# Optimization experiments

Hardware: AMD Instinct MI355X
Metric: run time of the kernel (lower is better)

## Reference

```python
import jax, jax.numpy as jnp
import numpy as np

STRIDE = 1

def setup_inputs() -> dict:
    key = jax.random.key(0)
    k1, k2 = jax.random.split(key)
    x = jax.random.normal(k1, (16, 32, 32768), dtype=jnp.float32)
    # original uses torch.rand -> uniform [0,1)
    kernel = jax.random.uniform(k2, (1, 32, 32, 3), dtype=jnp.float32)
    return {"x": x, "kernel": kernel}

def reference(x, kernel):
    # Faithful intent of the module: strided valid 1D convolution.
    # x: (B, C_in, L); kernel: (1, C_out, C_in, K)
    w = kernel[0]  # (C_out, C_in, K)
    out = jax.lax.conv_general_dilated(
        x, w,
        window_strides=(STRIDE,),
        padding='VALID',
        dimension_numbers=('NCH', 'OIH', 'NCH'),
    )  # (B, C_out, (L-K)//STRIDE + 1)
    return out
```

## Files before the change

### kernel.cpp

```cpp
#include <hip/hip_runtime.h>

#define L_IN   32768
#define L_OUT  32766
#define C_IN   32
#define C_OUT  32
#define KW     3
#define TILE_L 256
#define XROW   260
#define NTILES 128

__global__ void transpose_w(const float* __restrict__ w, float* __restrict__ wt) {
    int i = blockIdx.x * 256 + threadIdx.x;
    if (i < C_IN * C_OUT * KW) {
        int g  = i / 768;
        int r  = i - g * 768;
        int ci = r / 24;
        int t  = r - ci * 24;
        int cl = t / 3;
        int k  = t - cl * 3;
        wt[i] = w[(g * 8 + cl) * (C_IN * KW) + ci * KW + k];
    }
}

__global__ __launch_bounds__(256, 4) void conv1d_hybrid(
    const float* __restrict__ x, const float* __restrict__ wt,
    float* __restrict__ out)
{
    __shared__ __attribute__((aligned(16))) float xs[C_IN * XROW];

    const int tid       = threadIdx.x;
    const int lane      = tid & 63;
    const int w         = tid >> 6;
    const int blk       = blockIdx.x;
    const int b         = blk >> 7;
    const int tile      = blk & (NTILES - 1);
    const int tile_base = tile << 8;

    const float* xb = x + (size_t)b * C_IN * L_IN;

#pragma unroll
    for (int r = 0; r < 8; ++r) {
        const int row = w * 8 + r;
        const float* src = xb + (size_t)row * L_IN + tile_base + lane * 4;
        __builtin_amdgcn_global_load_lds(
            (const __attribute__((address_space(1))) void*)src,
            (__attribute__((address_space(3))) void*)&xs[row * XROW],
            16, 0, 0);
    }

    if (tid < C_IN) {
        float2 h = make_float2(0.f, 0.f);
        if (tile_base + 257 < L_IN)
            h = *(const float2*)(xb + (size_t)tid * L_IN + tile_base + 256);
        xs[tid * XROW + 256] = h.x;
        xs[tid * XROW + 257] = h.y;
    }
    __syncthreads();

    const int g  = __builtin_amdgcn_readfirstlane(w);
    const int l0 = lane * 4;

    float acc[8][4];
#pragma unroll
    for (int c = 0; c < 8; ++c)
#pragma unroll
        for (int j = 0; j < 4; ++j) acc[c][j] = 0.f;

    const float* xp = &xs[l0];
    const float* wr = wt + g * (C_IN * 24);

#pragma unroll 4
    for (int ci = 0; ci < C_IN; ++ci) {
        float xv[6];
        float4 xa = *(const float4*)(xp);
        float2 xc = *(const float2*)(xp + 4);
        xv[0] = xa.x; xv[1] = xa.y; xv[2] = xa.z; xv[3] = xa.w;
        xv[4] = xc.x; xv[5] = xc.y;

        float wv[24];
#pragma unroll
        for (int q = 0; q < 6; ++q) {
            float4 t = *(const float4*)(wr + q * 4);
            wv[q*4+0] = t.x; wv[q*4+1] = t.y; wv[q*4+2] = t.z; wv[q*4+3] = t.w;
        }

#pragma unroll
        for (int c = 0; c < 8; ++c)
#pragma unroll
            for (int j = 0; j < 4; ++j)
#pragma unroll
                for (int k = 0; k < KW; ++k)
                    acc[c][j] = fmaf(wv[c * KW + k], xv[j + k], acc[c][j]);

        xp += XROW;
        wr += 24;
    }

    const int lg = tile_base + l0;
    float* ob = out + ((size_t)b * C_OUT + g * 8) * L_OUT + lg;
#pragma unroll
    for (int c = 0; c < 8; ++c) {
        *(float2*)(ob) = make_float2(acc[c][0], acc[c][1]);
        if (lg + 3 < L_OUT)
            *(float2*)(ob + 2) = make_float2(acc[c][2], acc[c][3]);
        else if (lg + 2 < L_OUT)
            ob[2] = acc[c][2];
        ob += L_OUT;
    }
}

extern "C" void kernel_launch(void* const* d_in, const int* in_sizes, int n_in,
                              void* d_out, int out_size, void* d_ws, size_t ws_size,
                              hipStream_t stream) {
    const float* x = (const float*)d_in[0];
    const float* w = (const float*)d_in[1];
    float* out     = (float*)d_out;
    float* wt      = (float*)d_ws;

    transpose_w<<<dim3(12), 256, 0, stream>>>(w, wt);
    conv1d_hybrid<<<dim3(16 * NTILES), 256, 0, stream>>>(x, wt, out);
}
```

Before: 133.1 us.

## Replace FP32 FMA conv with split-bf16 MFMA (3-pass) and smaller tiles

Rewrites the conv inner loop to use bf16 MFMA 16x16x32 instructions. Inputs and weights are split into hi/lo bf16 pairs and three MFMA products are summed to approximate fp32 accuracy. The input tile is converted and transposed into LDS in a channel-contiguous layout, and the tile length is halved so each block covers 128 outputs. This is meant to move the compute off the vector FMA units onto matrix cores. In exchange it adds conversion work and scalar global loads, drops the direct global-to-LDS load path, uses uncoalesced-looking strided output stores, and slightly lowers precision.

```diff
diff --git a/kernel.cpp b/kernel.cpp
--- a/kernel.cpp
+++ b/kernel.cpp
@@ -5,107 +5,134 @@
 #define C_IN   32
 #define C_OUT  32
 #define KW     3
-#define TILE_L 256
-#define XROW   260
-#define NTILES 128
+#define TILE_L 128
+#define NTILES 256
+#define PITCH  40
+#define XROWS  (TILE_L + 2)
 
-__global__ void transpose_w(const float* __restrict__ w, float* __restrict__ wt) {
-    int i = blockIdx.x * 256 + threadIdx.x;
-    if (i < C_IN * C_OUT * KW) {
-        int g  = i / 768;
-        int r  = i - g * 768;
-        int ci = r / 24;
-        int t  = r - ci * 24;
-        int cl = t / 3;
-        int k  = t - cl * 3;
-        wt[i] = w[(g * 8 + cl) * (C_IN * KW) + ci * KW + k];
-    }
+typedef __attribute__((ext_vector_type(8))) short bf16x8;
+typedef __attribute__((ext_vector_type(4))) float f32x4;
+
+__device__ __forceinline__ unsigned short bf16_rne(float f) {
+    unsigned u = __float_as_uint(f);
+    u += 0x7fffu + ((u >> 16) & 1u);
+    return (unsigned short)(u >> 16);
+}
+__device__ __forceinline__ float bf16_to_f32(unsigned short h) {
+    return __uint_as_float(((unsigned)h) << 16);
 }
 
-__global__ __launch_bounds__(256, 4) void conv1d_hybrid(
-    const float* __restrict__ x, const float* __restrict__ wt,
+__global__ void prep_w(const float* __restrict__ w, unsigned short* __restrict__ wtf) {
+    const int i = blockIdx.x * 256 + threadIdx.x;
+    if (i >= 6 * 64 * 8) return;
+    const int f    = i >> 9;
+    const int rr   = i & 511;
+    const int lane = rr >> 3;
+    const int j    = rr & 7;
+    const int kw   = f >> 1;
+    const int cot  = f & 1;
+    const int co   = cot * 16 + (lane & 15);
+    const int ci   = (lane >> 4) * 8 + j;
+    const float v  = w[(co * C_IN + ci) * KW + kw];
+    const unsigned short hi = bf16_rne(v);
+    const unsigned short lo = bf16_rne(v - bf16_to_f32(hi));
+    wtf[(f * 64 + lane) * 16 + j]     = hi;
+    wtf[(f * 64 + lane) * 16 + 8 + j] = lo;
+}
+
+__global__ __launch_bounds__(256, 4) void conv1d_mfma(
+    const float* __restrict__ x, const unsigned short* __restrict__ wtf,
     float* __restrict__ out)
 {
-    __shared__ __attribute__((aligned(16))) float xs[C_IN * XROW];
+    __shared__ __attribute__((aligned(16))) unsigned short xh[XROWS * PITCH];
+    __shared__ __attribute__((aligned(16))) unsigned short xl[XROWS * PITCH];
 
-    const int tid       = threadIdx.x;
-    const int lane      = tid & 63;
-    const int w         = tid >> 6;
-    const int blk       = blockIdx.x;
-    const int b         = blk >> 7;
-    const int tile      = blk & (NTILES - 1);
-    const int tile_base = tile << 8;
+    const int tid  = threadIdx.x;
+    const int lane = tid & 63;
+    const int wv   = tid >> 6;
+    const int bb   = blockIdx.x >> 8;
+    const int tile = blockIdx.x & (NTILES - 1);
+    const int l0   = tile * TILE_L;
 
-    const float* xb = x + (size_t)b * C_IN * L_IN;
+    const float* xb = x + ((size_t)bb * C_IN) * L_IN + l0;
 
+    bf16x8 wah[6], wal[6];
 #pragma unroll
-    for (int r = 0; r < 8; ++r) {
-        const int row = w * 8 + r;
-        const float* src = xb + (size_t)row * L_IN + tile_base + lane * 4;
-        __builtin_amdgcn_global_load_lds(
-            (const __attribute__((address_space(1))) void*)src,
-            (__attribute__((address_space(3))) void*)&xs[row * XROW],
-            16, 0, 0);
+    for (int f = 0; f < 6; ++f) {
+        const bf16x8* p = (const bf16x8*)(wtf + (f * 64 + lane) * 16);
+        wah[f] = p[0];
+        wal[f] = p[1];
     }
 
-    if (tid < C_IN) {
-        float2 h = make_float2(0.f, 0.f);
-        if (tile_base + 257 < L_IN)
-            h = *(const float2*)(xb + (size_t)tid * L_IN + tile_base + 256);
-        xs[tid * XROW + 256] = h.x;
-        xs[tid * XROW + 257] = h.y;
+    {
+        const int c    = tid & 31;
+        const int rrow = tid >> 5;
+#pragma unroll
+        for (int r = 0; r < 4; ++r) {
+            const int ci = rrow + r * 8;
+            const float* src = xb + (size_t)ci * L_IN;
+#pragma unroll
+            for (int q = 0; q < 4; ++q) {
+                const int l = c + q * 32;
+                const float v = src[l];
+                const unsigned short hi = bf16_rne(v);
+                const unsigned short lo = bf16_rne(v - bf16_to_f32(hi));
+                xh[l * PITCH + ci] = hi;
+                xl[l * PITCH + ci] = lo;
+            }
+        }
+    }
+    if (tid < 64) {
+        const int h  = tid & 1;
+        const int ci = tid >> 1;
+        const int gl = l0 + TILE_L + h;
+        float v = 0.f;
+        if (gl < L_IN) v = xb[(size_t)ci * L_IN + TILE_L + h];
+        const unsigned short hi = bf16_rne(v);
+        const unsigned short lo = bf16_rne(v - bf16_to_f32(hi));
+        xh[(TILE_L + h) * PITCH + ci] = hi;
+        xl[(TILE_L + h) * PITCH + ci] = lo;
     }
     __syncthreads();
 
-    const int g  = __builtin_amdgcn_readfirstlane(w);
-    const int l0 = lane * 4;
+    const int n  = lane & 15;
+    const int kg = lane >> 4;
+    const int lb = wv * 32;
 
-    float acc[8][4];
-#pragma unroll
-    for (int c = 0; c < 8; ++c)
-#pragma unroll
-        for (int j = 0; j < 4; ++j) acc[c][j] = 0.f;
-
-    const float* xp = &xs[l0];
-    const float* wr = wt + g * (C_IN * 24);
-
-#pragma unroll 4
-    for (int ci = 0; ci < C_IN; ++ci) {
-        float xv[6];
-        float4 xa = *(const float4*)(xp);
-        float2 xc = *(const float2*)(xp + 4);
-        xv[0] = xa.x; xv[1] = xa.y; xv[2] = xa.z; xv[3] = xa.w;
-        xv[4] = xc.x; xv[5] = xc.y;
-
-        float wv[24];
-#pragma unroll
-        for (int q = 0; q < 6; ++q) {
-            float4 t = *(const float4*)(wr + q * 4);
-            wv[q*4+0] = t.x; wv[q*4+1] = t.y; wv[q*4+2] = t.z; wv[q*4+3] = t.w;
-        }
+    f32x4 acc[2][2] = {{{0.f,0.f,0.f,0.f},{0.f,0.f,0.f,0.f}},
+                       {{0.f,0.f,0.f,0.f},{0.f,0.f,0.f,0.f}}};
 
 #pragma unroll
-        for (int c = 0; c < 8; ++c)
+    for (int kw = 0; kw < KW; ++kw) {
 #pragma unroll
-            for (int j = 0; j < 4; ++j)
+        for (int lt = 0; lt < 2; ++lt) {
+            const int lrow = lb + lt * 16 + n + kw;
+            const bf16x8 bh = *(const bf16x8*)&xh[lrow * PITCH + kg * 8];
+            const bf16x8 bl = *(const bf16x8*)&xl[lrow * PITCH + kg * 8];
 #pragma unroll
-                for (int k = 0; k < KW; ++k)
-                    acc[c][j] = fmaf(wv[c * KW + k], xv[j + k], acc[c][j]);
-
-        xp += XROW;
-        wr += 24;
+            for (int cot = 0; cot < 2; ++cot) {
+                const int f = kw * 2 + cot;
+                acc[cot][lt] = __builtin_amdgcn_mfma_f32_16x16x32_bf16(wah[f], bh, acc[cot][lt], 0, 0, 0);
+                acc[cot][lt] = __builtin_amdgcn_mfma_f32_16x16x32_bf16(wah[f], bl, acc[cot][lt], 0, 0, 0);
+                acc[cot][lt] = __builtin_amdgcn_mfma_f32_16x16x32_bf16(wal[f], bh, acc[cot][lt], 0, 0, 0);
+            }
+        }
     }
 
-    const int lg = tile_base + l0;
-    float* ob = out + ((size_t)b * C_OUT + g * 8) * L_OUT + lg;
+    float* ob = out + (size_t)bb * C_OUT * L_OUT;
+    const int lw = l0 + lb;
 #pragma unroll
-    for (int c = 0; c < 8; ++c) {
-        *(float2*)(ob) = make_float2(acc[c][0], acc[c][1]);
-        if (lg + 3 < L_OUT)
-            *(float2*)(ob + 2) = make_float2(acc[c][2], acc[c][3]);
-        else if (lg + 2 < L_OUT)
-            ob[2] = acc[c][2];
-        ob += L_OUT;
+    for (int cot = 0; cot < 2; ++cot) {
+#pragma unroll
+        for (int lt = 0; lt < 2; ++lt) {
+            const int l = lw + lt * 16 + n;
+            if (l < L_OUT) {
+                float* op = ob + (size_t)(cot * 16 + kg * 4) * L_OUT + l;
+#pragma unroll
+                for (int r = 0; r < 4; ++r)
+                    op[(size_t)r * L_OUT] = acc[cot][lt][r];
+            }
+        }
     }
 }
 
@@ -115,8 +142,8 @@
     const float* x = (const float*)d_in[0];
     const float* w = (const float*)d_in[1];
     float* out     = (float*)d_out;
-    float* wt      = (float*)d_ws;
+    unsigned short* wtf = (unsigned short*)d_ws;
 
-    transpose_w<<<dim3(12), 256, 0, stream>>>(w, wt);
-    conv1d_hybrid<<<dim3(16 * NTILES), 256, 0, stream>>>(x, wt, out);
+    prep_w<<<dim3(12), 256, 0, stream>>>(w, wtf);
+    conv1d_mfma<<<dim3(16 * NTILES), 256, 0, stream>>>(x, wtf, out);
 }
```

Measured after the change: 126.5 us. 1.05x faster.
